# Kernel tuning notes

Hardware: AMD Instinct MI355X
Metric: run time of the kernel (lower is better)

## Reference

```python
import jax, jax.numpy as jnp
import numpy as np

L, N, E = 2048, 8, 1024
H = 16
KP = 256
KSZ = L // KP  # conv kernel size and stride = 8


def setup_inputs() -> dict:
    key = jax.random.key(0)
    ks = jax.random.split(key, 10)
    s = 0.02
    return {
        "query": jax.random.normal(ks[0], (L, N, E), jnp.float32),
        "key": jax.random.normal(ks[1], (L, N, E), jnp.float32),
        "value": jax.random.normal(ks[2], (L, N, E), jnp.float32),
        "in_proj_w": jax.random.normal(ks[3], (3 * E, E), jnp.float32) * s,
        "in_proj_b": jnp.zeros((3 * E,), jnp.float32),
        "e_w": jax.random.normal(ks[4], (E, E, KSZ), jnp.float32) * s,  # Conv1d OIH
        "e_b": jnp.zeros((E,), jnp.float32),
        "f_w": jax.random.normal(ks[5], (E, E, KSZ), jnp.float32) * s,
        "f_b": jnp.zeros((E,), jnp.float32),
        "out_w": jax.random.normal(ks[6], (E, E), jnp.float32) * s,
        "out_b": jnp.zeros((E,), jnp.float32),
    }


def _compress(x, w, b):
    # x: (S, N, E) -> conv1d over seq with kernel=stride=KSZ -> (Kp, N, E)
    xc = jnp.transpose(x, (1, 2, 0))  # (N, E, S)
    y = jax.lax.conv_general_dilated(
        xc, w, window_strides=(KSZ,), padding="VALID",
        dimension_numbers=("NCH", "OIH", "NCH"))
    y = y + b[None, :, None]
    return jnp.transpose(y, (2, 0, 1))  # (Kp, N, E)


def reference(query, key, value, in_proj_w, in_proj_b, e_w, e_b, f_w, f_b, out_w, out_b):
    D = E // H
    scaling = D ** -0.5
    q = query @ in_proj_w[:E].T + in_proj_b[:E]
    k = key @ in_proj_w[E:2 * E].T + in_proj_b[E:2 * E]
    v = value @ in_proj_w[2 * E:].T + in_proj_b[2 * E:]
    q = q * scaling
    k = _compress(k, e_w, e_b)  # (Kp, N, E)
    v = _compress(v, f_w, f_b)
    Kp = k.shape[0]
    # reshape to (N*H, len, D)
    qh = jnp.transpose(q.reshape(L, N * H, D), (1, 0, 2))
    kh = jnp.transpose(k.reshape(Kp, N * H, D), (1, 0, 2))
    vh = jnp.transpose(v.reshape(Kp, N * H, D), (1, 0, 2))
    attn = jax.nn.softmax(jnp.einsum("bld,bkd->blk", qh, kh), axis=-1)
    out = jnp.einsum("blk,bkd->bld", attn, vh)  # (N*H, L, D)
    out = jnp.transpose(out, (1, 0, 2)).reshape(L, N, E)
    out = out @ out_w.T + out_b
    attn_weights = attn.reshape(N, H, L, Kp).mean(axis=1)  # need_weights avg over heads
    return out, attn_weights
```

## Files before the change

kernel.cpp:

```cpp
#include <hip/hip_runtime.h>

typedef unsigned short u16;
typedef u16  u16x4 __attribute__((ext_vector_type(4)));
typedef u16  u16x8 __attribute__((ext_vector_type(8)));
typedef float f32x4 __attribute__((ext_vector_type(4)));
typedef int   i32x4 __attribute__((ext_vector_type(4)));
typedef __bf16 bf16x8 __attribute__((ext_vector_type(8)));

#define LSEQ 2048
#define NB 8
#define EDIM 1024
#define HNUM 16
#define DDIM 64
#define KPDIM 256
#define NE (NB*EDIM)
#define MROWS (LSEQ*NB)
#define AWSZ ((size_t)NB*LSEQ*KPDIM)

__device__ __forceinline__ u16 f2b(float f) {
  unsigned u = __builtin_bit_cast(unsigned, f);
  u += 0x7fffu + ((u >> 16) & 1u);
  return (u16)(u >> 16);
}

__device__ __forceinline__ void gl_lds16(const void* g, void* l) {
  __builtin_amdgcn_global_load_lds(
      (const __attribute__((address_space(1))) void*)g,
      (__attribute__((address_space(3))) void*)l, 16, 0, 0);
}

__device__ __forceinline__ f32x4 mfma16(bf16x8 a, bf16x8 b, f32x4 c) {
  return __builtin_amdgcn_mfma_f32_16x16x32_bf16(a, b, c, 0, 0, 0);
}

#define BAR()   __builtin_amdgcn_s_barrier()
#define LGKM0() asm volatile("s_waitcnt lgkmcnt(0)" ::: "memory")
#define WVM6()  asm volatile("s_waitcnt vmcnt(6)" ::: "memory")
#define WVM0()  asm volatile("s_waitcnt vmcnt(0)" ::: "memory")

__global__ void wconv(const float* __restrict__ src, u16* __restrict__ dst,
                      int n4, int scale_n4, float sc) {
  int i = blockIdx.x * blockDim.x + threadIdx.x;
  if (i >= n4) return;
  f32x4 v = ((const f32x4*)src)[i];
  float s = (i < scale_n4) ? sc : 1.0f;
  u16x4 o;
  o[0] = f2b(v[0] * s); o[1] = f2b(v[1] * s);
  o[2] = f2b(v[2] * s); o[3] = f2b(v[3] * s);
  ((u16x4*)dst)[i] = o;
}

__global__ void wtrans(const float* __restrict__ ew, const float* __restrict__ fw,
                       u16* __restrict__ eT, u16* __restrict__ fT) {
  const float* src = blockIdx.y ? fw : ew;
  u16* dst = blockIdx.y ? fT : eT;
  int eo = blockIdx.x >> 4;
  int ei0 = (blockIdx.x & 15) * 64;
  int l = threadIdx.x;
  __shared__ u16 lds[8][64];
  const float* s = src + (size_t)eo * 8192 + (size_t)ei0 * 8 + l * 8;
  f32x4 a = *(const f32x4*)s;
  f32x4 b = *(const f32x4*)(s + 4);
  float v[8] = {a[0], a[1], a[2], a[3], b[0], b[1], b[2], b[3]};
#pragma unroll
  for (int t = 0; t < 8; ++t) lds[t][l] = f2b(v[t]);
  __syncthreads();
  int t = l >> 3, c = l & 7;
  i32x4 out = *(const i32x4*)&lds[t][c * 8];
  *(i32x4*)(dst + (size_t)eo * 8192 + t * 1024 + ei0 + c * 8) = out;
}

__global__ void bscale(const float* __restrict__ b, float* __restrict__ out) {
  int i = blockIdx.x * blockDim.x + threadIdx.x;
  if (i < EDIM) out[i] = b[i] * 0.125f;
}

__global__ void castqkv(const float* __restrict__ q, const float* __restrict__ k,
                        const float* __restrict__ v, u16* __restrict__ out) {
  const float* src = blockIdx.y == 0 ? q : (blockIdx.y == 1 ? k : v);
  size_t base = (size_t)blockIdx.y * ((size_t)MROWS * EDIM);
  size_t i = ((size_t)blockIdx.x * 256 + threadIdx.x) * 8;
  f32x4 v0 = *(const f32x4*)(src + i);
  f32x4 v1 = *(const f32x4*)(src + i + 4);
  u16x8 o;
  o[0] = f2b(v0[0]); o[1] = f2b(v0[1]); o[2] = f2b(v0[2]); o[3] = f2b(v0[3]);
  o[4] = f2b(v1[0]); o[5] = f2b(v1[1]); o[6] = f2b(v1[2]); o[7] = f2b(v1[3]);
  *(u16x8*)(out + base + i) = o;
}

__global__ void redc(const float* __restrict__ part, const float* __restrict__ eb,
                     const float* __restrict__ fb, u16* __restrict__ kc,
                     u16* __restrict__ vcT) {
  int zc = blockIdx.y;
  const float* p = part + (size_t)zc * 4 * 2048 * 1024;
  const float* bias = zc ? fb : eb;
  size_t i = ((size_t)blockIdx.x * 256 + threadIdx.x) * 4;
  f32x4 s = *(const f32x4*)(p + i);
  s += *(const f32x4*)(p + 2097152 + i);
  s += *(const f32x4*)(p + 2 * 2097152 + i);
  s += *(const f32x4*)(p + 3 * 2097152 + i);
  int e = (int)(i & 1023);
  int row = (int)(i >> 10);
  int n = row >> 8, pp = row & 255;
  int h = e >> 6, d = e & 63;
  f32x4 b = *(const f32x4*)(bias + e);
  if (zc == 0) {
    u16x4 o;
    o[0] = f2b(s[0] + b[0]); o[1] = f2b(s[1] + b[1]);
    o[2] = f2b(s[2] + b[2]); o[3] = f2b(s[3] + b[3]);
    *(u16x4*)(kc + (((size_t)(n * HNUM + h) * KPDIM + pp) * DDIM + d)) = o;
  } else {
    size_t base = (size_t)(n * HNUM + h) * (DDIM * KPDIM);
#pragma unroll
    for (int q = 0; q < 4; ++q) {
      int dq = d + q;
      vcT[base + dq * 256 + (((pp >> 3) ^ (dq & 7)) * 8) + (pp & 7)] =
          f2b(s[q] + b[q]);
    }
  }
}

__global__ void awred(const float* __restrict__ awp, float* __restrict__ aw) {
  size_t i = ((size_t)blockIdx.x * 256 + threadIdx.x) * 4;
  f32x4 s = *(const f32x4*)(awp + i);
  s += *(const f32x4*)(awp + AWSZ + i);
  s += *(const f32x4*)(awp + 2 * AWSZ + i);
  s += *(const f32x4*)(awp + 3 * AWSZ + i);
  *(f32x4*)(aw + i) = s;
}

template<int AMODE, int OUTMODE>
__global__ __launch_bounds__(512, 2)
void gemm256(const void* A0p, const void* A1p, const void* A2p,
             const u16* B0p, const u16* B1p, const u16* B2p,
             const float* b0p, const float* b1p, const float* b2p,
             void* C0p, void* C1p, void* C2p,
             int M, int K, int kspl) {
  const int zc = blockIdx.z / kspl, sp = blockIdx.z % kspl;
  const void* Ap = zc == 0 ? A0p : (zc == 1 ? A1p : A2p);
  const u16* Bp = zc == 0 ? B0p : (zc == 1 ? B1p : B2p);
  const float* biasp = zc == 0 ? b0p : (zc == 1 ? b1p : b2p);
  void* Cp = zc == 0 ? C0p : (zc == 1 ? C1p : C2p);

  __shared__ u16 lds[2][2][2][128 * 64];

  const int tid = threadIdx.x;
  const int w = tid >> 6, lane = tid & 63;
  const int lr = lane & 15, lg = lane >> 4;
  const int wr = w >> 2, wc = w & 3;
  const int m0 = blockIdx.x * 256, n0 = blockIdx.y * 256;
  const int kper = K / kspl, kbase = sp * kper, nt = kper >> 6;

  f32x4 acc[8][4];
#pragma unroll
  for (int mi = 0; mi < 8; ++mi)
#pragma unroll
    for (int ni = 0; ni < 4; ++ni) {
      f32x4 zv = {0.f, 0.f, 0.f, 0.f};
      acc[mi][ni] = zv;
    }

  auto stage_half = [&](int buf, int op, int half, int kt) {
    const int k0 = kbase + (kt << 6);
#pragma unroll
    for (int i = 0; i < 2; ++i) {
      int c = i * 512 + tid;
      int r = c >> 3, j = c & 7, js = j ^ (r & 7);
      int row = half * 128 + r;
      u16* dst = &lds[buf][op][half][c * 8];
      if (op == 1) {
        gl_lds16(Bp + (size_t)(n0 + row) * K + k0 + js * 8, dst);
      } else if (AMODE == 0) {
        gl_lds16((const u16*)Ap + (size_t)(m0 + row) * K + k0 + js * 8, dst);
      } else {
        int m = m0 + row;
        int nn = m >> 8, p = m & 255;
        int k = k0 + js * 8;
        gl_lds16((const u16*)Ap + (size_t)(p * 8 + (k >> 10)) * NE +
                 nn * EDIM + (k & 1023), dst);
      }
    }
  };

  auto LDA = [&](int buf, int row, int ks) -> bf16x8 {
    return *(const bf16x8*)&lds[buf][0][row >> 7]
        [(row & 127) * 64 + (((ks * 4 + lg) ^ (row & 7)) << 3)];
  };
  auto LDB = [&](int buf, int row, int ks) -> bf16x8 {
    return *(const bf16x8*)&lds[buf][1][row >> 7]
        [(row & 127) * 64 + (((ks * 4 + lg) ^ (row & 7)) << 3)];
  };

  stage_half(0, 0, 0, 0); stage_half(0, 1, 0, 0);
  stage_half(0, 1, 1, 0); stage_half(0, 0, 1, 0);
  if (nt > 1) {
    stage_half(1, 1, 0, 1); stage_half(1, 1, 1, 1); stage_half(1, 0, 0, 1);
    WVM6();
  } else {
    WVM0();
  }
  BAR();

  for (int t = 0; t < nt; t += 2) {
    bf16x8 a0[4][2], a1[4][2], b0f[2][2], b1f[2][2];
#pragma unroll
    for (int mi = 0; mi < 4; ++mi)
#pragma unroll
      for (int ks = 0; ks < 2; ++ks)
        a0[mi][ks] = LDA(0, wr * 128 + mi * 16 + lr, ks);
#pragma unroll
    for (int ni = 0; ni < 2; ++ni)
#pragma unroll
      for (int ks = 0; ks < 2; ++ks)
        b0f[ni][ks] = LDB(0, wc * 64 + ni * 16 + lr, ks);
    stage_half(1, 0, 1, t + 1);
    BAR(); LGKM0();
    __builtin_amdgcn_s_setprio(1);
#pragma unroll
    for (int mi = 0; mi < 4; ++mi)
#pragma unroll
      for (int ni = 0; ni < 2; ++ni)
#pragma unroll
        for (int ks = 0; ks < 2; ++ks)
          acc[mi][ni] = mfma16(a0[mi][ks], b0f[ni][ks], acc[mi][ni]);
    __builtin_amdgcn_s_setprio(0);
    BAR();
#pragma unroll
    for (int ni = 0; ni < 2; ++ni)
#pragma unroll
      for (int ks = 0; ks < 2; ++ks)
        b1f[ni][ks] = LDB(0, wc * 64 + (ni + 2) * 16 + lr, ks);
    BAR(); LGKM0();
    __builtin_amdgcn_s_setprio(1);
#pragma unroll
    for (int mi = 0; mi < 4; ++mi)
#pragma unroll
      for (int ni = 0; ni < 2; ++ni)
#pragma unroll
        for (int ks = 0; ks < 2; ++ks)
          acc[mi][ni + 2] = mfma16(a0[mi][ks], b1f[ni][ks], acc[mi][ni + 2]);
    __builtin_amdgcn_s_setprio(0);
    BAR();
#pragma unroll
    for (int mi = 0; mi < 4; ++mi)
#pragma unroll
      for (int ks = 0; ks < 2; ++ks)
        a1[mi][ks] = LDA(0, wr * 128 + 64 + mi * 16 + lr, ks);
    if (t + 2 < nt) stage_half(0, 1, 0, t + 2);
    BAR(); LGKM0();
    __builtin_amdgcn_s_setprio(1);
#pragma unroll
    for (int mi = 0; mi < 4; ++mi)
#pragma unroll
      for (int ni = 0; ni < 2; ++ni)
#pragma unroll
        for (int ks = 0; ks < 2; ++ks)
          acc[mi + 4][ni + 2] = mfma16(a1[mi][ks], b1f[ni][ks], acc[mi + 4][ni + 2]);
    __builtin_amdgcn_s_setprio(0);
    BAR();
    if (t + 2 < nt) { stage_half(0, 1, 1, t + 2); stage_half(0, 0, 0, t + 2); }
    BAR();
    __builtin_amdgcn_s_setprio(1);
#pragma unroll
    for (int mi = 0; mi < 4; ++mi)
#pragma unroll
      for (int ni = 0; ni < 2; ++ni)
#pragma unroll
        for (int ks = 0; ks < 2; ++ks)
          acc[mi + 4][ni] = mfma16(a1[mi][ks], b0f[ni][ks], acc[mi + 4][ni]);
    __builtin_amdgcn_s_setprio(0);
    if (t + 2 < nt) { WVM6(); } else { WVM0(); }
    BAR();
#pragma unroll
    for (int mi = 0; mi < 4; ++mi)
#pragma unroll
      for (int ks = 0; ks < 2; ++ks)
        a0[mi][ks] = LDA(1, wr * 128 + mi * 16 + lr, ks);
#pragma unroll
    for (int ni = 0; ni < 2; ++ni)
#pragma unroll
      for (int ks = 0; ks < 2; ++ks)
        b0f[ni][ks] = LDB(1, wc * 64 + ni * 16 + lr, ks);
    if (t + 2 < nt) stage_half(0, 0, 1, t + 2);
    BAR(); LGKM0();
    __builtin_amdgcn_s_setprio(1);
#pragma unroll
    for (int mi = 0; mi < 4; ++mi)
#pragma unroll
      for (int ni = 0; ni < 2; ++ni)
#pragma unroll
        for (int ks = 0; ks < 2; ++ks)
          acc[mi][ni] = mfma16(a0[mi][ks], b0f[ni][ks], acc[mi][ni]);
    __builtin_amdgcn_s_setprio(0);
    BAR();
#pragma unroll
    for (int ni = 0; ni < 2; ++ni)
#pragma unroll
      for (int ks = 0; ks < 2; ++ks)
        b1f[ni][ks] = LDB(1, wc * 64 + (ni + 2) * 16 + lr, ks);
    BAR(); LGKM0();
    __builtin_amdgcn_s_setprio(1);
#pragma unroll
    for (int mi = 0; mi < 4; ++mi)
#pragma unroll
      for (int ni = 0; ni < 2; ++ni)
#pragma unroll
        for (int ks = 0; ks < 2; ++ks)
          acc[mi][ni + 2] = mfma16(a0[mi][ks], b1f[ni][ks], acc[mi][ni + 2]);
    __builtin_amdgcn_s_setprio(0);
    BAR();
#pragma unroll
    for (int mi = 0; mi < 4; ++mi)
#pragma unroll
      for (int ks = 0; ks < 2; ++ks)
        a1[mi][ks] = LDA(1, wr * 128 + 64 + mi * 16 + lr, ks);
    if (t + 3 < nt) stage_half(1, 1, 0, t + 3);
    BAR(); LGKM0();
    __builtin_amdgcn_s_setprio(1);
#pragma unroll
    for (int mi = 0; mi < 4; ++mi)
#pragma unroll
      for (int ni = 0; ni < 2; ++ni)
#pragma unroll
        for (int ks = 0; ks < 2; ++ks)
          acc[mi + 4][ni + 2] = mfma16(a1[mi][ks], b1f[ni][ks], acc[mi + 4][ni + 2]);
    __builtin_amdgcn_s_setprio(0);
    BAR();
    if (t + 3 < nt) { stage_half(1, 1, 1, t + 3); stage_half(1, 0, 0, t + 3); }
    BAR();
    __builtin_amdgcn_s_setprio(1);
#pragma unroll
    for (int mi = 0; mi < 4; ++mi)
#pragma unroll
      for (int ni = 0; ni < 2; ++ni)
#pragma unroll
        for (int ks = 0; ks < 2; ++ks)
          acc[mi + 4][ni] = mfma16(a1[mi][ks], b0f[ni][ks], acc[mi + 4][ni]);
    __builtin_amdgcn_s_setprio(0);
    if (t + 3 < nt) { WVM6(); } else { WVM0(); }
    BAR();
  }

  if (OUTMODE == 0) {
    __syncthreads();
    u16* cw = (u16*)&lds[0][0][0][0];
#pragma unroll
    for (int ni = 0; ni < 4; ++ni) {
      const int col = wc * 64 + ni * 16 + lr;
      const float bv = biasp[n0 + col];
#pragma unroll
      for (int mi = 0; mi < 8; ++mi)
#pragma unroll
        for (int j = 0; j < 4; ++j) {
          const int row = wr * 128 + mi * 16 + lg * 4 + j;
          cw[row * 256 + col] = f2b(acc[mi][ni][j] + bv);
        }
    }
    __syncthreads();
#pragma unroll
    for (int it = 0; it < 16; ++it) {
      int c = it * 512 + tid;
      int row = c >> 5, ch = c & 31;
      i32x4 v = *(const i32x4*)&cw[row * 256 + ch * 8];
      *(i32x4*)((u16*)Cp + (size_t)(m0 + row) * 1024 + n0 + ch * 8) = v;
    }
  } else {
#pragma unroll
    for (int ni = 0; ni < 4; ++ni) {
      const int col = n0 + wc * 64 + ni * 16 + lr;
      const float bv = (OUTMODE == 2) ? 0.f : biasp[col];
#pragma unroll
      for (int mi = 0; mi < 8; ++mi)
#pragma unroll
        for (int j = 0; j < 4; ++j) {
          const int row = m0 + wr * 128 + mi * 16 + lg * 4 + j;
          const float v = acc[mi][ni][j] + bv;
          if (OUTMODE == 2)
            ((float*)Cp)[(size_t)sp * M * 1024 + (size_t)row * 1024 + col] = v;
          else
            ((float*)Cp)[(size_t)row * 1024 + col] = v;
        }
    }
  }
}

template<int AMODE, int OUTMODE>
__global__ __launch_bounds__(256)
void gemm_bt(const void* A0p, const void* A1p, const void* A2p,
             const u16* B0p, const u16* B1p, const u16* B2p,
             const float* b0p, const float* b1p, const float* b2p,
             void* C0p, void* C1p, void* C2p,
             int M, int K, int kspl) {
  const int zc = blockIdx.z / kspl;
  const int sp = blockIdx.z % kspl;
  const void* Ap = zc == 0 ? A0p : (zc == 1 ? A1p : A2p);
  const u16* Bp = zc == 0 ? B0p : (zc == 1 ? B1p : B2p);
  const float* biasp = zc == 0 ? b0p : (zc == 1 ? b1p : b2p);
  void* Cp = zc == 0 ? C0p : (zc == 1 ? C1p : C2p);

  __shared__ u16 Alds[128 * 64];
  __shared__ u16 Blds[128 * 64];

  const int tid = threadIdx.x;
  const int w = tid >> 6, lane = tid & 63;
  const int lr = lane & 15, lg = lane >> 4;
  const int m0 = blockIdx.x * 128, n0 = blockIdx.y * 128;
  const int wr = (w >> 1) * 64, wc = (w & 1) * 64;
  const int brow = lane >> 3;
  const int bcol = (lane & 7) * 8;

  f32x4 acc[4][4];
#pragma unroll
  for (int mi = 0; mi < 4; ++mi)
#pragma unroll
    for (int ni = 0; ni < 4; ++ni) {
      f32x4 zv = {0.f, 0.f, 0.f, 0.f};
      acc[mi][ni] = zv;
    }

  const int kper = K / kspl;
  const int ktn = kper >> 6;
  const int kb = sp * kper;
  for (int kt = 0; kt < ktn; ++kt) {
    const int k0 = kb + (kt << 6);
    __syncthreads();
#pragma unroll
    for (int i = 0; i < 4; ++i) {
      const int c = w * 4 + i;
      const int row = c * 8 + brow;
      gl_lds16(Bp + (size_t)(n0 + row) * K + k0 + bcol, &Blds[c * 512]);
    }
    if (AMODE == 2) {
      const float* Af = (const float*)Ap;
#pragma unroll
      for (int i = 0; i < 4; ++i) {
        const int c = i * 256 + tid;
        const int row = c >> 3, k8 = (c & 7) * 8;
        const float* s = Af + (size_t)(m0 + row) * K + k0 + k8;
        f32x4 v0 = *(const f32x4*)s;
        f32x4 v1 = *(const f32x4*)(s + 4);
        u16x8 pk;
        pk[0] = f2b(v0[0]); pk[1] = f2b(v0[1]); pk[2] = f2b(v0[2]); pk[3] = f2b(v0[3]);
        pk[4] = f2b(v1[0]); pk[5] = f2b(v1[1]); pk[6] = f2b(v1[2]); pk[7] = f2b(v1[3]);
        *(u16x8*)&Alds[row * 64 + k8] = pk;
      }
    } else if (AMODE == 0) {
      const u16* Ab = (const u16*)Ap;
#pragma unroll
      for (int i = 0; i < 4; ++i) {
        const int c = w * 4 + i;
        const int row = c * 8 + brow;
        gl_lds16(Ab + (size_t)(m0 + row) * K + k0 + bcol, &Alds[c * 512]);
      }
    } else {
      const u16* Ab = (const u16*)Ap;
#pragma unroll
      for (int i = 0; i < 4; ++i) {
        const int c = w * 4 + i;
        const int m = m0 + c * 8 + brow;
        const int nn = m >> 8, p = m & 255;
        const int k = k0 + bcol;
        gl_lds16(Ab + (size_t)(p * 8 + (k >> 10)) * NE + nn * EDIM + (k & 1023),
                 &Alds[c * 512]);
      }
    }
    __syncthreads();
#pragma unroll
    for (int ks = 0; ks < 2; ++ks) {
      bf16x8 af[4], bf[4];
#pragma unroll
      for (int mi = 0; mi < 4; ++mi)
        af[mi] = *(const bf16x8*)&Alds[(wr + mi * 16 + lr) * 64 + ks * 32 + lg * 8];
#pragma unroll
      for (int ni = 0; ni < 4; ++ni)
        bf[ni] = *(const bf16x8*)&Blds[(wc + ni * 16 + lr) * 64 + ks * 32 + lg * 8];
#pragma unroll
      for (int mi = 0; mi < 4; ++mi)
#pragma unroll
        for (int ni = 0; ni < 4; ++ni)
          acc[mi][ni] = mfma16(af[mi], bf[ni], acc[mi][ni]);
    }
  }
#pragma unroll
  for (int ni = 0; ni < 4; ++ni) {
    const int col = n0 + wc + ni * 16 + lr;
    const float bv = (OUTMODE == 2) ? 0.f : biasp[col];
#pragma unroll
    for (int mi = 0; mi < 4; ++mi)
#pragma unroll
      for (int j = 0; j < 4; ++j) {
        const int row = m0 + wr + mi * 16 + lg * 4 + j;
        const float v = acc[mi][ni][j] + bv;
        if (OUTMODE == 4) {
          const int nn = row >> 8, pp = row & 255, h = col >> 6, d = col & 63;
          ((u16*)Cp)[(size_t)(nn * HNUM + h) * (DDIM * KPDIM) + d * 256 +
                     (((pp >> 3) ^ (d & 7)) * 8) + (pp & 7)] = f2b(v);
        } else if (OUTMODE == 3) {
          const int nn = row >> 8, pp = row & 255, h = col >> 6, d = col & 63;
          ((u16*)Cp)[((size_t)(nn * HNUM + h) * KPDIM + pp) * DDIM + d] = f2b(v);
        } else if (OUTMODE == 2)
          ((float*)Cp)[(size_t)sp * M * 1024 + (size_t)row * 1024 + col] = v;
        else if (OUTMODE == 1)
          ((float*)Cp)[(size_t)row * 1024 + col] = v;
        else
          ((u16*)Cp)[(size_t)row * 1024 + col] = f2b(v);
      }
  }
}

__global__ __launch_bounds__(256)
void attn_fused(const u16* __restrict__ Q, const u16* __restrict__ Kc,
                const u16* __restrict__ VcT, u16* __restrict__ Aout,
                float* __restrict__ AWp, int hpg) {
  __shared__ u16 Ares[256 * 64];
  __shared__ u16 Bres[64 * 256];
  const int tid = threadIdx.x;
  const int w = tid >> 6, lane = tid & 63;
  const int lr = lane & 15, lg = lane >> 4;
  const int n = blockIdx.y;
  const int l0 = blockIdx.x * 64;
  const int lrow = l0 + w * 16 + lr;
  char* kbase = (char*)Ares;
  char* vbase = (char*)Bres;
  char* pbase = (char*)Ares + w * 8192;

  f32x4 macc[16];
#pragma unroll
  for (int ni = 0; ni < 16; ++ni) { f32x4 zv = {0.f,0.f,0.f,0.f}; macc[ni] = zv; }

  for (int hh = 0; hh < hpg; ++hh) {
    const int h = blockIdx.z * hpg + hh;
    const u16* kh = Kc + (size_t)(n * HNUM + h) * (KPDIM * DDIM);
    const u16* vh = VcT + (size_t)(n * HNUM + h) * (DDIM * KPDIM);
    __syncthreads();
#pragma unroll
    for (int it = 0; it < 8; ++it) {
      int c = it * 256 + tid;
      int p = c >> 3, j = c & 7;
      gl_lds16(kh + p * 64 + ((j ^ (p & 7)) << 3), kbase + c * 16);
    }
#pragma unroll
    for (int it = 0; it < 8; ++it) {
      int c = it * 256 + tid;
      gl_lds16(vh + c * 8, vbase + c * 16);
    }
    const u16* qp = Q + (size_t)lrow * NE + n * EDIM + h * DDIM + lg * 8;
    bf16x8 aq0 = *(const bf16x8*)qp;
    bf16x8 aq1 = *(const bf16x8*)(qp + 32);
    __syncthreads();
    f32x4 s[16];
#pragma unroll
    for (int ni = 0; ni < 16; ++ni) { f32x4 zv = {0.f,0.f,0.f,0.f}; s[ni] = zv; }
#pragma unroll
    for (int ni = 0; ni < 16; ++ni) {
      int row = ni * 16 + lr;
      const char* kr = kbase + row * 128;
      bf16x8 b0 = *(const bf16x8*)(kr + ((lg ^ (row & 7)) << 4));
      bf16x8 b1 = *(const bf16x8*)(kr + (((4 + lg) ^ (row & 7)) << 4));
      s[ni] = mfma16(aq0, b0, s[ni]);
      s[ni] = mfma16(aq1, b1, s[ni]);
    }
    float mx[4], sm[4], inv[4];
#pragma unroll
    for (int j = 0; j < 4; ++j) mx[j] = -1e30f;
#pragma unroll
    for (int ni = 0; ni < 16; ++ni)
#pragma unroll
      for (int j = 0; j < 4; ++j) mx[j] = fmaxf(mx[j], s[ni][j]);
#pragma unroll
    for (int msk = 1; msk <= 8; msk <<= 1)
#pragma unroll
      for (int j = 0; j < 4; ++j) mx[j] = fmaxf(mx[j], __shfl_xor(mx[j], msk, 64));
#pragma unroll
    for (int j = 0; j < 4; ++j) sm[j] = 0.f;
#pragma unroll
    for (int ni = 0; ni < 16; ++ni)
#pragma unroll
      for (int j = 0; j < 4; ++j) {
        float e = __expf(s[ni][j] - mx[j]);
        s[ni][j] = e; sm[j] += e;
      }
#pragma unroll
    for (int msk = 1; msk <= 8; msk <<= 1)
#pragma unroll
      for (int j = 0; j < 4; ++j) sm[j] += __shfl_xor(sm[j], msk, 64);
#pragma unroll
    for (int j = 0; j < 4; ++j) inv[j] = 1.0f / sm[j];
    __syncthreads();
#pragma unroll
    for (int ni = 0; ni < 16; ++ni)
#pragma unroll
      for (int j = 0; j < 4; ++j) {
        float pv = s[ni][j] * inv[j];
        macc[ni][j] += pv * 0.0625f;
        int r = lg * 4 + j;
        *(u16*)(pbase + r * 512 + ((ni * 32 + lr * 2) ^ ((r & 7) << 4))) = f2b(pv);
      }
    f32x4 o[4];
#pragma unroll
    for (int ni2 = 0; ni2 < 4; ++ni2) { f32x4 zv = {0.f,0.f,0.f,0.f}; o[ni2] = zv; }
#pragma unroll
    for (int ks = 0; ks < 8; ++ks) {
      bf16x8 a = *(const bf16x8*)(pbase + lr * 512 + ((ks * 64 + 16 * lg) ^ ((lr & 7) << 4)));
#pragma unroll
      for (int ni2 = 0; ni2 < 4; ++ni2) {
        int d = ni2 * 16 + lr;
        bf16x8 b = *(const bf16x8*)(vbase + d * 512 + (((ks * 4 + lg) ^ (d & 7)) << 4));
        o[ni2] = mfma16(a, b, o[ni2]);
      }
    }
#pragma unroll
    for (int ni2 = 0; ni2 < 4; ++ni2)
#pragma unroll
      for (int j = 0; j < 4; ++j) {
        int gl = l0 + w * 16 + lg * 4 + j;
        Aout[(size_t)gl * NE + n * EDIM + h * DDIM + ni2 * 16 + lr] = f2b(o[ni2][j]);
      }
  }
  float* awo = AWp + (size_t)blockIdx.z * AWSZ + (size_t)n * (LSEQ * KPDIM);
#pragma unroll
  for (int ni = 0; ni < 16; ++ni)
#pragma unroll
    for (int j = 0; j < 4; ++j) {
      int r = lg * 4 + j;
      awo[(size_t)(l0 + w * 16 + r) * KPDIM + ni * 16 + lr] = macc[ni][j];
    }
}

extern "C" void kernel_launch(void* const* d_in, const int* in_sizes, int n_in,
                              void* d_out, int out_size, void* d_ws, size_t ws_size,
                              hipStream_t stream) {
  const float* query = (const float*)d_in[0];
  const float* key   = (const float*)d_in[1];
  const float* value = (const float*)d_in[2];
  const float* ipw   = (const float*)d_in[3];
  const float* ipb   = (const float*)d_in[4];
  const float* ew    = (const float*)d_in[5];
  const float* eb    = (const float*)d_in[6];
  const float* fw    = (const float*)d_in[7];
  const float* fb    = (const float*)d_in[8];
  const float* ow    = (const float*)d_in[9];
  const float* ob    = (const float*)d_in[10];

  char* ws = (char*)d_ws;
  size_t off = 0;
  auto alloc = [&](size_t bytes) {
    void* p = ws + off;
    off += (bytes + 255) & ~(size_t)255;
    return p;
  };
  u16* qp    = (u16*)alloc((size_t)MROWS * EDIM * 2);
  u16* kp    = (u16*)alloc((size_t)MROWS * EDIM * 2);
  u16* vp    = (u16*)alloc((size_t)MROWS * EDIM * 2);
  u16* ao    = (u16*)alloc((size_t)MROWS * EDIM * 2);
  u16* kc    = (u16*)alloc((size_t)NB * KPDIM * EDIM * 2);
  u16* vcT   = (u16*)alloc((size_t)NB * KPDIM * EDIM * 2);
  u16* w_in  = (u16*)alloc((size_t)3 * EDIM * EDIM * 2);
  u16* w_eT  = (u16*)alloc((size_t)EDIM * 8 * EDIM * 2);
  u16* w_fT  = (u16*)alloc((size_t)EDIM * 8 * EDIM * 2);
  u16* w_out = (u16*)alloc((size_t)EDIM * EDIM * 2);
  float* bq  = (float*)alloc(EDIM * 4);
  size_t base_needed = off;

  size_t qkv16_b = (size_t)3 * MROWS * EDIM * 2;
  size_t part_b  = (size_t)2 * 4 * 2048 * 1024 * 4;
  bool bigX  = ws_size >= base_needed + qkv16_b;
  bool midX  = ws_size >= base_needed + part_b;
  char* X = (char*)alloc(bigX ? qkv16_b : (midX ? part_b : 0));
  u16* qkv16 = (u16*)X;
  float* part = (float*)X;
  float* awp  = (float*)X;

  float* out_f = (float*)d_out;
  float* aw_f  = (float*)d_out + (size_t)MROWS * EDIM;

  wconv<<<dim3(3072), 256, 0, stream>>>(ipw, w_in, 786432, 262144, 0.125f);
  wconv<<<dim3(1024), 256, 0, stream>>>(ow, w_out, 262144, 0, 1.0f);
  wtrans<<<dim3(16384, 2), 64, 0, stream>>>(ew, fw, w_eT, w_fT);
  bscale<<<dim3(4), 256, 0, stream>>>(ipb, bq);

  if (bigX) {
    castqkv<<<dim3(8192, 3), 256, 0, stream>>>(query, key, value, qkv16);
    gemm256<0, 0><<<dim3(64, 4, 3), 512, 0, stream>>>(
        qkv16, qkv16 + (size_t)MROWS * EDIM, qkv16 + (size_t)2 * MROWS * EDIM,
        w_in, w_in + 1048576, w_in + 2097152,
        bq, ipb + 1024, ipb + 2048,
        qp, kp, vp, MROWS, 1024, 1);
  } else {
    gemm_bt<2, 0><<<dim3(128, 8, 3), 256, 0, stream>>>(
        query, key, value,
        w_in, w_in + 1048576, w_in + 2097152,
        bq, ipb + 1024, ipb + 2048,
        qp, kp, vp, MROWS, 1024, 1);
  }

  if (bigX || midX) {
    gemm256<1, 2><<<dim3(8, 4, 8), 512, 0, stream>>>(
        kp, vp, vp,
        w_eT, w_fT, w_fT,
        eb, fb, fb,
        part, part + (size_t)4 * 2048 * 1024, part,
        NB * KPDIM, 8192, 4);
    redc<<<dim3(2048, 2), 256, 0, stream>>>(part, eb, fb, kc, vcT);
  } else {
    gemm_bt<1, 3><<<dim3(16, 8, 1), 256, 0, stream>>>(
        kp, kp, kp, w_eT, w_eT, w_eT, eb, eb, eb,
        kc, kc, kc, NB * KPDIM, 8192, 1);
    gemm_bt<1, 4><<<dim3(16, 8, 1), 256, 0, stream>>>(
        vp, vp, vp, w_fT, w_fT, w_fT, fb, fb, fb,
        vcT, vcT, vcT, NB * KPDIM, 8192, 1);
  }

  if (bigX) {
    attn_fused<<<dim3(32, 8, 4), 256, 0, stream>>>(qp, kc, vcT, ao, awp, 4);
    awred<<<dim3(4096), 256, 0, stream>>>(awp, aw_f);
  } else {
    attn_fused<<<dim3(32, 8, 1), 256, 0, stream>>>(qp, kc, vcT, ao, aw_f, 16);
  }

  gemm256<0, 1><<<dim3(64, 4, 1), 512, 0, stream>>>(
      ao, ao, ao,
      w_out, w_out, w_out,
      ob, ob, ob,
      out_f, out_f, out_f, MROWS, 1024, 1);
}
```

Measured before the change: 437.9 us.

## Add double-buffered attention kernel that prefetches K/V for the next heads

Adds attn_fused4, a version of the fused attention kernel specialised to four heads per block. It double-buffers K and V in LDS through async global-to-LDS loads, so the next head's tiles arrive while the current head's softmax and PV MFMAs run. All four heads' Q fragments are preloaded into registers. It doubles LDS use, which can lower occupancy, and it relies on hand-placed vmcnt waits and barriers that must match the prefetch pattern exactly.

```diff
diff --git a/kernel.cpp b/kernel.cpp
--- a/kernel.cpp
+++ b/kernel.cpp
@@ -34,7 +34,9 @@
 }
 
 #define BAR()   __builtin_amdgcn_s_barrier()
+#define SB0()   __builtin_amdgcn_sched_barrier(0)
 #define LGKM0() asm volatile("s_waitcnt lgkmcnt(0)" ::: "memory")
+#define WVM16() asm volatile("s_waitcnt vmcnt(16)" ::: "memory")
 #define WVM6()  asm volatile("s_waitcnt vmcnt(6)" ::: "memory")
 #define WVM0()  asm volatile("s_waitcnt vmcnt(0)" ::: "memory")
 
@@ -509,6 +511,146 @@
 }
 
 __global__ __launch_bounds__(256)
+void attn_fused4(const u16* __restrict__ Q, const u16* __restrict__ Kc,
+                 const u16* __restrict__ VcT, u16* __restrict__ Aout,
+                 float* __restrict__ AWp) {
+  __shared__ u16 Kbuf[2][256 * 64];
+  __shared__ u16 Vbuf[2][64 * 256];
+  const int tid = threadIdx.x;
+  const int w = tid >> 6, lane = tid & 63;
+  const int lr = lane & 15, lg = lane >> 4;
+  const int n = blockIdx.y;
+  const int l0 = blockIdx.x * 64;
+  const int lrow = l0 + w * 16 + lr;
+  const int h0 = blockIdx.z * 4;
+
+  auto stageKV = [&](int b, int hh) {
+    const int h = h0 + hh;
+    const u16* kh = Kc + (size_t)(n * HNUM + h) * (KPDIM * DDIM);
+    const u16* vh = VcT + (size_t)(n * HNUM + h) * (DDIM * KPDIM);
+    char* kb = (char*)Kbuf[b];
+    char* vb = (char*)Vbuf[b];
+#pragma unroll
+    for (int it = 0; it < 8; ++it) {
+      int c = it * 256 + tid, p = c >> 3, j = c & 7;
+      gl_lds16(kh + p * 64 + ((j ^ (p & 7)) << 3), kb + c * 16);
+    }
+#pragma unroll
+    for (int it = 0; it < 8; ++it) {
+      int c = it * 256 + tid;
+      gl_lds16(vh + c * 8, vb + c * 16);
+    }
+  };
+
+  bf16x8 aq[4][2];
+#pragma unroll
+  for (int hh = 0; hh < 4; ++hh) {
+    const u16* qp = Q + (size_t)lrow * NE + n * EDIM + (h0 + hh) * DDIM + lg * 8;
+    aq[hh][0] = *(const bf16x8*)qp;
+    aq[hh][1] = *(const bf16x8*)(qp + 32);
+  }
+  stageKV(0, 0);
+  stageKV(1, 1);
+  WVM16();
+  BAR(); SB0();
+
+  f32x4 macc[16];
+#pragma unroll
+  for (int ni = 0; ni < 16; ++ni) { f32x4 zv = {0.f,0.f,0.f,0.f}; macc[ni] = zv; }
+
+#pragma unroll
+  for (int hh = 0; hh < 4; ++hh) {
+    const int b = hh & 1;
+    const int h = h0 + hh;
+    char* kbase = (char*)Kbuf[b];
+    char* vbase = (char*)Vbuf[b];
+    char* pbase = (char*)Kbuf[b] + w * 8192;
+    f32x4 s[16];
+#pragma unroll
+    for (int ni = 0; ni < 16; ++ni) { f32x4 zv = {0.f,0.f,0.f,0.f}; s[ni] = zv; }
+#pragma unroll
+    for (int ni = 0; ni < 16; ++ni) {
+      int row = ni * 16 + lr;
+      const char* kr = kbase + row * 128;
+      bf16x8 b0 = *(const bf16x8*)(kr + ((lg ^ (row & 7)) << 4));
+      bf16x8 b1 = *(const bf16x8*)(kr + (((4 + lg) ^ (row & 7)) << 4));
+      s[ni] = mfma16(aq[hh][0], b0, s[ni]);
+      s[ni] = mfma16(aq[hh][1], b1, s[ni]);
+    }
+    float mx[4], sm[4], inv[4], invs[4];
+#pragma unroll
+    for (int j = 0; j < 4; ++j) mx[j] = -1e30f;
+#pragma unroll
+    for (int ni = 0; ni < 16; ++ni)
+#pragma unroll
+      for (int j = 0; j < 4; ++j) mx[j] = fmaxf(mx[j], s[ni][j]);
+#pragma unroll
+    for (int msk = 1; msk <= 8; msk <<= 1)
+#pragma unroll
+      for (int j = 0; j < 4; ++j) mx[j] = fmaxf(mx[j], __shfl_xor(mx[j], msk, 64));
+#pragma unroll
+    for (int j = 0; j < 4; ++j) sm[j] = 0.f;
+#pragma unroll
+    for (int ni = 0; ni < 16; ++ni)
+#pragma unroll
+      for (int j = 0; j < 4; ++j) {
+        float e = __expf(s[ni][j] - mx[j]);
+        s[ni][j] = e; sm[j] += e;
+      }
+#pragma unroll
+    for (int msk = 1; msk <= 8; msk <<= 1)
+#pragma unroll
+      for (int j = 0; j < 4; ++j) sm[j] += __shfl_xor(sm[j], msk, 64);
+#pragma unroll
+    for (int j = 0; j < 4; ++j) { inv[j] = 1.0f / sm[j]; invs[j] = inv[j] * 0.0625f; }
+    BAR(); SB0();
+#pragma unroll
+    for (int ni = 0; ni < 16; ++ni)
+#pragma unroll
+      for (int j = 0; j < 4; ++j) {
+        macc[ni][j] += s[ni][j] * invs[j];
+        int r = lg * 4 + j;
+        *(u16*)(pbase + r * 512 + ((ni * 32 + lr * 2) ^ ((r & 7) << 4))) =
+            f2b(s[ni][j]);
+      }
+    f32x4 o[4];
+#pragma unroll
+    for (int ni2 = 0; ni2 < 4; ++ni2) { f32x4 zv = {0.f,0.f,0.f,0.f}; o[ni2] = zv; }
+#pragma unroll
+    for (int ks = 0; ks < 8; ++ks) {
+      bf16x8 a = *(const bf16x8*)(pbase + lr * 512 + ((ks * 64 + 16 * lg) ^ ((lr & 7) << 4)));
+#pragma unroll
+      for (int ni2 = 0; ni2 < 4; ++ni2) {
+        int d = ni2 * 16 + lr;
+        bf16x8 bv = *(const bf16x8*)(vbase + d * 512 + (((ks * 4 + lg) ^ (d & 7)) << 4));
+        o[ni2] = mfma16(a, bv, o[ni2]);
+      }
+    }
+#pragma unroll
+    for (int ni2 = 0; ni2 < 4; ++ni2)
+#pragma unroll
+      for (int j = 0; j < 4; ++j) {
+        int gl = l0 + w * 16 + lg * 4 + j;
+        Aout[(size_t)gl * NE + n * EDIM + h * DDIM + ni2 * 16 + lr] =
+            f2b(o[ni2][j] * inv[j]);
+      }
+    if (hh < 3) {
+      WVM16();
+      BAR(); SB0();
+      if (hh < 2) stageKV(b, hh + 2);
+    }
+  }
+  float* awo = AWp + (size_t)blockIdx.z * AWSZ + (size_t)n * (LSEQ * KPDIM);
+#pragma unroll
+  for (int ni = 0; ni < 16; ++ni)
+#pragma unroll
+    for (int j = 0; j < 4; ++j) {
+      int r = lg * 4 + j;
+      awo[(size_t)(l0 + w * 16 + r) * KPDIM + ni * 16 + lr] = macc[ni][j];
+    }
+}
+
+__global__ __launch_bounds__(256)
 void attn_fused(const u16* __restrict__ Q, const u16* __restrict__ Kc,
                 const u16* __restrict__ VcT, u16* __restrict__ Aout,
                 float* __restrict__ AWp, int hpg) {
@@ -712,7 +854,7 @@
   }
 
   if (bigX) {
-    attn_fused<<<dim3(32, 8, 4), 256, 0, stream>>>(qp, kc, vcT, ao, awp, 4);
+    attn_fused4<<<dim3(32, 8, 4), 256, 0, stream>>>(qp, kc, vcT, ao, awp);
     awred<<<dim3(4096), 256, 0, stream>>>(awp, aw_f);
   } else {
     attn_fused<<<dim3(32, 8, 1), 256, 0, stream>>>(qp, kc, vcT, ao, aw_f, 16);
```

Result: slower. 498.1 us (+13.8%).
